# Kernel optimization log

Measured on AMD Instinct MI355X. Metric: run time of the kernel, lower is better.

Reference implementation:

```python
import jax, jax.numpy as jnp
import numpy as np
import math

EMBED_DIM = 512
NUM_HEADS = 8
B, T = 1, 4096

def setup_inputs() -> dict:
    key = jax.random.key(0)
    ks = jax.random.split(key, 12)
    D = EMBED_DIM
    s = 1.0 / math.sqrt(D)
    inp = {
        "x": jax.random.normal(ks[0], (B, T, D), dtype=jnp.float32),
        "ln1_scale": jnp.ones((D,), jnp.float32),
        "ln1_bias": jnp.zeros((D,), jnp.float32),
        "Wq": jax.random.normal(ks[1], (D, D), jnp.float32) * s,
        "bq": jnp.zeros((D,), jnp.float32),
        "Wk": jax.random.normal(ks[2], (D, D), jnp.float32) * s,
        "bk": jnp.zeros((D,), jnp.float32),
        "Wv": jax.random.normal(ks[3], (D, D), jnp.float32) * s,
        "bv": jnp.zeros((D,), jnp.float32),
        "Wo": jax.random.normal(ks[4], (D, D), jnp.float32) * s,
        "bo": jnp.zeros((D,), jnp.float32),
        "ln2_scale": jnp.ones((D,), jnp.float32),
        "ln2_bias": jnp.zeros((D,), jnp.float32),
        "W1": jax.random.normal(ks[5], (D, 4 * D), jnp.float32) * s,
        "b1": jnp.zeros((4 * D,), jnp.float32),
        "W2": jax.random.normal(ks[6], (4 * D, D), jnp.float32) * (1.0 / math.sqrt(4 * D)),
        "b2": jnp.zeros((D,), jnp.float32),
    }
    return inp

def _layernorm(x, scale, bias, eps=1e-6):
    mu = jnp.mean(x, axis=-1, keepdims=True)
    var = jnp.mean(jnp.square(x - mu), axis=-1, keepdims=True)
    return (x - mu) * jax.lax.rsqrt(var + eps) * scale + bias

def reference(x, ln1_scale, ln1_bias, Wq, bq, Wk, bk, Wv, bv, Wo, bo,
              ln2_scale, ln2_bias, W1, b1, W2, b2):
    Bb, Tt, D = x.shape
    H = NUM_HEADS
    hd = D // H
    residual = x
    h = _layernorm(x, ln1_scale, ln1_bias)
    q = (h @ Wq + bq).reshape(Bb, Tt, H, hd).transpose(0, 2, 1, 3)
    k = (h @ Wk + bk).reshape(Bb, Tt, H, hd).transpose(0, 2, 1, 3)
    v = (h @ Wv + bv).reshape(Bb, Tt, H, hd).transpose(0, 2, 1, 3)
    # [B,H,T,T] scores (naive attention as in the original module)
    scores = jnp.einsum('bhqd,bhkd->bhqk', q, k) / math.sqrt(hd)
    probs = jax.nn.softmax(scores, axis=-1)
    out = jnp.einsum('bhqk,bhkd->bhqd', probs, v).transpose(0, 2, 1, 3).reshape(Bb, Tt, D)
    h = out @ Wo + bo  # dropout deterministic -> identity
    x = h + residual
    residual = x
    h = _layernorm(x, ln2_scale, ln2_bias)
    h = jax.nn.gelu(h @ W1 + b1, approximate=True)
    h = h @ W2 + b2
    return h + residual
```

## Files before the change

kernel.cpp:

```cpp
#include <hip/hip_runtime.h>
#include <hip/hip_bf16.h>
#include <stdint.h>

typedef __bf16 bf16;
typedef __bf16 bf16x4 __attribute__((ext_vector_type(4)));
typedef __bf16 bf16x8 __attribute__((ext_vector_type(8)));
typedef float  f32x4  __attribute__((ext_vector_type(4)));
typedef float  f32x16 __attribute__((ext_vector_type(16)));

#define MFMA16(A_, B_, C_) __builtin_amdgcn_mfma_f32_16x16x32_bf16((A_), (B_), (C_), 0, 0, 0)
#define MFMA32(A_, B_, C_) __builtin_amdgcn_mfma_f32_32x32x16_bf16((A_), (B_), (C_), 0, 0, 0)

#define QSCALE 0.1803368801111137f

__device__ __forceinline__ void gload_lds16(const void* g, void* l) {
  __builtin_amdgcn_global_load_lds(
      (const __attribute__((address_space(1))) unsigned int*)g,
      (__attribute__((address_space(3))) unsigned int*)l, 16, 0, 0);
}

__device__ __forceinline__ unsigned pk2(float lo, float hi_) {
  union { bf16 h[2]; unsigned u; } t;
  t.h[0] = (bf16)lo; t.h[1] = (bf16)hi_;
  return t.u;
}

__device__ __forceinline__ float fast_exp2(float x) {
#if __has_builtin(__builtin_amdgcn_exp2f)
  return __builtin_amdgcn_exp2f(x);
#else
  return exp2f(x);
#endif
}

__global__ __launch_bounds__(256) void prep(const float* __restrict__ Wq,
                                            const float* __restrict__ Wk,
                                            const float* __restrict__ Wv,
                                            const float* __restrict__ Wo,
                                            const float* __restrict__ W1,
                                            const float* __restrict__ W2,
                                            const float* __restrict__ bq,
                                            const float* __restrict__ bk,
                                            const float* __restrict__ bv,
                                            bf16* __restrict__ wqkvT, bf16* __restrict__ woT,
                                            bf16* __restrict__ w1T, bf16* __restrict__ w2T,
                                            float* __restrict__ bqkv) {
  const int b = blockIdx.x;
  if (b >= 768) {
    int i = (b - 768) * 256 + threadIdx.x;
    if (i < 1536)
      bqkv[i] = (i < 512) ? bq[i] * QSCALE : (i < 1024 ? bk[i - 512] : bv[i - 1024]);
    return;
  }
  const float* in; bf16* outp; int K, N, t; float sc = 1.f;
  if (b < 64)       { in = Wq; outp = wqkvT;              K = 512;  N = 512;  t = b;       sc = QSCALE; }
  else if (b < 128) { in = Wk; outp = wqkvT + 512 * 512;  K = 512;  N = 512;  t = b - 64;  }
  else if (b < 192) { in = Wv; outp = wqkvT + 1024 * 512; K = 512;  N = 512;  t = b - 128; }
  else if (b < 256) { in = Wo; outp = woT;                K = 512;  N = 512;  t = b - 192; }
  else if (b < 512) { in = W1; outp = w1T;                K = 512;  N = 2048; t = b - 256; }
  else              { in = W2; outp = w2T;                K = 2048; N = 512;  t = b - 512; }
  const int tx = K >> 6;
  const int k0 = (t % tx) * 64, n0 = (t / tx) * 64;
  __shared__ bf16 tile[64][72];
  const int tid = threadIdx.x;
#pragma unroll
  for (int s = 0; s < 16; ++s) {
    int j = tid + s * 256;
    int r = j >> 6, c = j & 63;
    tile[r][c] = (bf16)(in[(size_t)(k0 + r) * N + n0 + c] * sc);
  }
  __syncthreads();
#pragma unroll
  for (int s = 0; s < 16; ++s) {
    int j = tid + s * 256;
    int n = j >> 6, k = j & 63;
    outp[(size_t)(n0 + n) * K + k0 + k] = tile[k][n];
  }
}

__global__ __launch_bounds__(256) void ln_k(const float* __restrict__ x,
                                            const float* __restrict__ sc,
                                            const float* __restrict__ bi,
                                            bf16* __restrict__ out) {
  const int w = threadIdx.x >> 6, l = threadIdx.x & 63;
  const int row = blockIdx.x * 4 + w;
  const float4* xp = (const float4*)(x + (size_t)row * 512 + l * 8);
  float4 v0 = xp[0], v1 = xp[1];
  float xv[8] = {v0.x, v0.y, v0.z, v0.w, v1.x, v1.y, v1.z, v1.w};
  float s = 0.f, q = 0.f;
#pragma unroll
  for (int j = 0; j < 8; ++j) { s += xv[j]; q += xv[j] * xv[j]; }
#pragma unroll
  for (int m = 1; m < 64; m <<= 1) { s += __shfl_xor(s, m); q += __shfl_xor(q, m); }
  const float mean = s * (1.f / 512.f);
  const float var = q * (1.f / 512.f) - mean * mean;
  const float rstd = rsqrtf(var + 1e-6f);
  const float4* scp = (const float4*)(sc + l * 8);
  const float4* bip = (const float4*)(bi + l * 8);
  float4 s0 = scp[0], s1 = scp[1], b0 = bip[0], b1 = bip[1];
  float sv[8] = {s0.x, s0.y, s0.z, s0.w, s1.x, s1.y, s1.z, s1.w};
  float bv[8] = {b0.x, b0.y, b0.z, b0.w, b1.x, b1.y, b1.z, b1.w};
  bf16x8 ov;
#pragma unroll
  for (int j = 0; j < 8; ++j) ov[j] = (bf16)((xv[j] - mean) * rstd * sv[j] + bv[j]);
  *(bf16x8*)(out + (size_t)row * 512 + l * 8) = ov;
}

__global__ __launch_bounds__(256) void ln2_comb(const float* __restrict__ p0,
                                                const float* __restrict__ p1,
                                                const float* __restrict__ x,
                                                const float* __restrict__ bo,
                                                const float* __restrict__ sc,
                                                const float* __restrict__ bi,
                                                float* __restrict__ x2,
                                                bf16* __restrict__ h2) {
  const int w = threadIdx.x >> 6, l = threadIdx.x & 63;
  const int row = blockIdx.x * 4 + w;
  const size_t base = (size_t)row * 512 + l * 8;
  float xv[8];
#pragma unroll
  for (int j = 0; j < 2; ++j) {
    float4 a = *(const float4*)(p0 + base + j * 4);
    float4 b = *(const float4*)(p1 + base + j * 4);
    float4 c = *(const float4*)(x + base + j * 4);
    float4 d = *(const float4*)(bo + l * 8 + j * 4);
    xv[j * 4 + 0] = a.x + b.x + c.x + d.x;
    xv[j * 4 + 1] = a.y + b.y + c.y + d.y;
    xv[j * 4 + 2] = a.z + b.z + c.z + d.z;
    xv[j * 4 + 3] = a.w + b.w + c.w + d.w;
  }
  *(float4*)(x2 + base) = make_float4(xv[0], xv[1], xv[2], xv[3]);
  *(float4*)(x2 + base + 4) = make_float4(xv[4], xv[5], xv[6], xv[7]);
  float s = 0.f, q = 0.f;
#pragma unroll
  for (int j = 0; j < 8; ++j) { s += xv[j]; q += xv[j] * xv[j]; }
#pragma unroll
  for (int m = 1; m < 64; m <<= 1) { s += __shfl_xor(s, m); q += __shfl_xor(q, m); }
  const float mean = s * (1.f / 512.f);
  const float var = q * (1.f / 512.f) - mean * mean;
  const float rstd = rsqrtf(var + 1e-6f);
  const float4* scp = (const float4*)(sc + l * 8);
  const float4* bip = (const float4*)(bi + l * 8);
  float4 s0 = scp[0], s1 = scp[1], b0 = bip[0], b1 = bip[1];
  float sv[8] = {s0.x, s0.y, s0.z, s0.w, s1.x, s1.y, s1.z, s1.w};
  float bv[8] = {b0.x, b0.y, b0.z, b0.w, b1.x, b1.y, b1.z, b1.w};
  bf16x8 ov;
#pragma unroll
  for (int j = 0; j < 8; ++j) ov[j] = (bf16)((xv[j] - mean) * rstd * sv[j] + bv[j]);
  *(bf16x8*)(h2 + base) = ov;
}

__global__ __launch_bounds__(256) void final_comb(const float* __restrict__ parts, int nsplit,
                                                  const float* __restrict__ b2,
                                                  const float* __restrict__ x2,
                                                  float* __restrict__ outp) {
  const int i4 = blockIdx.x * 256 + threadIdx.x;
  const size_t off = (size_t)i4 * 4;
  float4 acc = *(const float4*)(x2 + off);
  float4 bb = *(const float4*)(b2 + (off & 511));
  acc.x += bb.x; acc.y += bb.y; acc.z += bb.z; acc.w += bb.w;
  for (int z = 0; z < nsplit; ++z) {
    float4 p = *(const float4*)(parts + (size_t)z * 4096 * 512 + off);
    acc.x += p.x; acc.y += p.y; acc.z += p.z; acc.w += p.w;
  }
  *(float4*)(outp + off) = acc;
}

template <int EPI>
__global__ __launch_bounds__(256) void gemm_bt(const bf16* __restrict__ A,
                                               const bf16* __restrict__ Bt,
                                               const float* __restrict__ bias,
                                               const float* __restrict__ res,
                                               void* __restrict__ outp,
                                               bf16* __restrict__ k2,
                                               bf16* __restrict__ v2,
                                               int M, int N, int K) {
  __shared__ bf16 a_lds[2][128 * 64];
  __shared__ bf16 b_lds[2][128 * 64];
  const int m0 = blockIdx.x * 128, n0 = blockIdx.y * 128;
  const int tid = threadIdx.x, l = tid & 63, w = tid >> 6;
  const int wm = w >> 1, wn = w & 1;
  const int lc = l & 15, g = l >> 4;
  const int srow = l >> 3;
  const int cs = (l & 7) ^ srow;

  const bf16* ag = A + (size_t)(m0 + w * 8 + srow) * K + cs * 8;
  const bf16* bg = Bt + (size_t)(n0 + w * 8 + srow) * K + cs * 8;
  const size_t rstep = (size_t)32 * K;

#define GSTAGE(B_)                                                       \
  do {                                                                   \
    _Pragma("unroll")                                                    \
    for (int r_ = 0; r_ < 4; ++r_) {                                     \
      gload_lds16(ag + r_ * rstep, (char*)a_lds[B_] + (r_ * 32 + w * 8) * 128); \
      gload_lds16(bg + r_ * rstep, (char*)b_lds[B_] + (r_ * 32 + w * 8) * 128); \
    }                                                                    \
    ag += 64; bg += 64;                                                  \
  } while (0)

  f32x4 acc[4][4] = {};
  const int kiters = K >> 6;
  GSTAGE(0);
  __syncthreads();
  for (int kt = 0; kt < kiters; ++kt) {
    const int cur = kt & 1;
    if (kt + 1 < kiters) GSTAGE(cur ^ 1);
    const bf16* ab = a_lds[cur];
    const bf16* bb2 = b_lds[cur];
#pragma unroll
    for (int kk = 0; kk < 2; ++kk) {
      bf16x8 af[4], bfr[4];
#pragma unroll
      for (int i = 0; i < 4; ++i) {
        const int sw = ((kk * 4 + g) ^ (lc & 7)) * 8;
        af[i]  = *(const bf16x8*)(ab + (wm * 64 + i * 16 + lc) * 64 + sw);
        bfr[i] = *(const bf16x8*)(bb2 + (wn * 64 + i * 16 + lc) * 64 + sw);
      }
#pragma unroll
      for (int mi = 0; mi < 4; ++mi)
#pragma unroll
        for (int ni = 0; ni < 4; ++ni)
          acc[mi][ni] = MFMA16(af[mi], bfr[ni], acc[mi][ni]);
    }
    __syncthreads();
  }
#undef GSTAGE

#pragma unroll
  for (int mi = 0; mi < 4; ++mi)
#pragma unroll
    for (int ni = 0; ni < 4; ++ni) {
      const int col = n0 + wn * 64 + ni * 16 + lc;
      const float bb = bias[col];
#pragma unroll
      for (int i = 0; i < 4; ++i) {
        const int row = m0 + wm * 64 + mi * 16 + g * 4 + i;
        float v = acc[mi][ni][i] + bb;
        if constexpr (EPI == 1) {
          ((float*)outp)[(size_t)row * N + col] = v + res[(size_t)row * N + col];
        } else if constexpr (EPI == 2) {
          float t = -2.3022077697f * (v + 0.044715f * v * v * v);
          float gl = v / (1.f + fast_exp2(t));
          ((bf16*)outp)[(size_t)row * N + col] = (bf16)gl;
        } else {
          const bf16 bv16 = (bf16)v;
          if (col < 512) {
            ((bf16*)outp)[(size_t)row * 512 + col] = bv16;
          } else if (col < 1024) {
            const int hd = (col - 512) >> 6, d = col & 63;
            k2[(size_t)hd * 262144 + (size_t)row * 64 + d] = bv16;
          } else {
            const int hd = (col - 1024) >> 6, d = col & 63;
            v2[(size_t)hd * 262144 + (size_t)(row >> 5) * 2048 + d * 32 + (row & 31)] = bv16;
          }
        }
      }
    }
}

__global__ __launch_bounds__(256) void gemm_skp(const bf16* __restrict__ A,
                                                const bf16* __restrict__ Bt,
                                                float* __restrict__ parts,
                                                int M, int N, int Kstride, int Kc) {
  __shared__ bf16 a_lds[2][128 * 64];
  __shared__ bf16 b_lds[2][128 * 64];
  const int m0 = blockIdx.x * 128, n0 = blockIdx.y * 128, kz = blockIdx.z;
  A += (size_t)kz * Kc;
  Bt += (size_t)kz * Kc;
  float* outp = parts + (size_t)kz * M * N;
  const int tid = threadIdx.x, l = tid & 63, w = tid >> 6;
  const int wm = w >> 1, wn = w & 1;
  const int lc = l & 15, g = l >> 4;
  const int srow = l >> 3;
  const int cs = (l & 7) ^ srow;

  const bf16* ag = A + (size_t)(m0 + w * 8 + srow) * Kstride + cs * 8;
  const bf16* bg = Bt + (size_t)(n0 + w * 8 + srow) * Kstride + cs * 8;
  const size_t rstep = (size_t)32 * Kstride;

#define GSTAGE(B_)                                                       \
  do {                                                                   \
    _Pragma("unroll")                                                    \
    for (int r_ = 0; r_ < 4; ++r_) {                                     \
      gload_lds16(ag + r_ * rstep, (char*)a_lds[B_] + (r_ * 32 + w * 8) * 128); \
      gload_lds16(bg + r_ * rstep, (char*)b_lds[B_] + (r_ * 32 + w * 8) * 128); \
    }                                                                    \
    ag += 64; bg += 64;                                                  \
  } while (0)

  f32x4 acc[4][4] = {};
  const int kiters = Kc >> 6;
  GSTAGE(0);
  __syncthreads();
  for (int kt = 0; kt < kiters; ++kt) {
    const int cur = kt & 1;
    if (kt + 1 < kiters) GSTAGE(cur ^ 1);
    const bf16* ab = a_lds[cur];
    const bf16* bb2 = b_lds[cur];
#pragma unroll
    for (int kk = 0; kk < 2; ++kk) {
      bf16x8 af[4], bfr[4];
#pragma unroll
      for (int i = 0; i < 4; ++i) {
        const int sw = ((kk * 4 + g) ^ (lc & 7)) * 8;
        af[i]  = *(const bf16x8*)(ab + (wm * 64 + i * 16 + lc) * 64 + sw);
        bfr[i] = *(const bf16x8*)(bb2 + (wn * 64 + i * 16 + lc) * 64 + sw);
      }
#pragma unroll
      for (int mi = 0; mi < 4; ++mi)
#pragma unroll
        for (int ni = 0; ni < 4; ++ni)
          acc[mi][ni] = MFMA16(af[mi], bfr[ni], acc[mi][ni]);
    }
    __syncthreads();
  }
#undef GSTAGE

#pragma unroll
  for (int mi = 0; mi < 4; ++mi)
#pragma unroll
    for (int ni = 0; ni < 4; ++ni) {
      const int col = n0 + wn * 64 + ni * 16 + lc;
#pragma unroll
      for (int i = 0; i < 4; ++i) {
        const int row = m0 + wm * 64 + mi * 16 + g * 4 + i;
        outp[(size_t)row * N + col] = acc[mi][ni][i];
      }
    }
}

__global__ __launch_bounds__(256, 4) void attn_k(const bf16* __restrict__ q2,
                                                 const bf16* __restrict__ k2,
                                                 const bf16* __restrict__ v2,
                                                 bf16* __restrict__ opart,
                                                 float* __restrict__ lpart) {
  const int bid = blockIdx.x;
  const int head = bid & 7;
  const int qt = (bid >> 3) & 63;
  const int ks = bid >> 9;
  const int w = threadIdx.x >> 6, l = threadIdx.x & 63;
  const int hi = l >> 5, l5 = l & 31;
  const int pair = w >> 1, wq = w & 1;

  __shared__ __align__(16) char smem[32768];
  char* kt_l = smem + pair * 16384;
  char* vt_l = kt_l + 8192;

  const int qrow0 = qt * 64 + wq * 32;
  const bf16* qb = q2 + (size_t)(qrow0 + l5) * 512 + head * 64;
  bf16x8 qf[4];
#pragma unroll
  for (int cc = 0; cc < 4; ++cc) qf[cc] = *(const bf16x8*)(qb + cc * 16 + hi * 8);

  const int kstart = ks * 2048 + pair * 1024;

  const int lr = l >> 3;
  const int lc3 = (l & 7) ^ lr;
  const char* kg = (const char*)k2 + (size_t)head * 524288 + (size_t)kstart * 128 +
                   (wq * 16 + lr) * 128 + lc3 * 16;
  const char* vg = (const char*)v2 + (size_t)head * 524288 + (size_t)(kstart >> 5) * 4096 +
                   (lc3 >> 2) * 2048 + (wq * 16 + lr) * 64 + (lc3 & 3) * 16;
  const int kdst = wq * 2048;

#define STAGE(B_)                                                            \
  do {                                                                       \
    gload_lds16(kg,        kt_l + (B_) * 4096 + kdst);                       \
    gload_lds16(kg + 1024, kt_l + (B_) * 4096 + kdst + 1024);                \
    gload_lds16(vg,        vt_l + (B_) * 4096 + kdst);                       \
    gload_lds16(vg + 512,  vt_l + (B_) * 4096 + kdst + 1024);                \
    kg += 4096; vg += 4096;                                                  \
  } while (0)

  STAGE(0);
  __syncthreads();

  f32x16 o0 = {}, o1 = {};
  float psum = 0.f;
  const int swl = l5 & 7;
  const char* kbase = kt_l + l5 * 128;
  const char* vbase = vt_l + l5 * 128;

  for (int t = 0; t < 32; ++t) {
    const int cur = t & 1;
    if (t < 31) STAGE(cur ^ 1);

    __builtin_amdgcn_s_setprio(1);
    f32x16 s = {};
#pragma unroll
    for (int cc = 0; cc < 4; ++cc) {
      bf16x8 kf = *(const bf16x8*)(kbase + cur * 4096 + ((cc * 2 + hi) ^ swl) * 16);
      s = MFMA32(kf, qf[cc], s);
    }
    __builtin_amdgcn_s_setprio(0);

#pragma unroll
    for (int c = 0; c < 2; ++c) {
      float p[8];
#pragma unroll
      for (int j = 0; j < 8; ++j) p[j] = fast_exp2(s[c * 8 + j]);
      psum += ((p[0] + p[1]) + (p[2] + p[3])) + ((p[4] + p[5]) + (p[6] + p[7]));
      unsigned X = pk2(p[0], p[1]), X2 = pk2(p[2], p[3]);
      unsigned Y = pk2(p[4], p[5]), Y2 = pk2(p[6], p[7]);
      asm volatile("v_permlane32_swap_b32 %0, %1" : "+v"(X), "+v"(Y));
      asm volatile("v_permlane32_swap_b32 %0, %1" : "+v"(X2), "+v"(Y2));
      union { unsigned wd[4]; bf16x8 v; } pa;
      pa.wd[0] = X; pa.wd[1] = X2; pa.wd[2] = Y; pa.wd[3] = Y2;
      bf16x8 vf0 = *(const bf16x8*)(vbase + cur * 4096 + ((c * 2 + hi) ^ swl) * 16);
      bf16x8 vf1 = *(const bf16x8*)(vbase + cur * 4096 + ((4 + c * 2 + hi) ^ swl) * 16);
      __builtin_amdgcn_s_setprio(1);
      o0 = MFMA32(vf0, pa.v, o0);
      o1 = MFMA32(vf1, pa.v, o1);
      __builtin_amdgcn_s_setprio(0);
    }
    __syncthreads();
  }
#undef STAGE

  float* comb = (float*)smem;
  if (w >= 2) {
    float* cb = comb + ((w - 2) * 64 + l) * 33;
#pragma unroll
    for (int r = 0; r < 16; ++r) { cb[r] = o0[r]; cb[16 + r] = o1[r]; }
    cb[32] = psum;
  }
  __syncthreads();
  if (w < 2) {
    const float* cb = comb + (w * 64 + l) * 33;
#pragma unroll
    for (int r = 0; r < 16; ++r) { o0[r] += cb[r]; o1[r] += cb[16 + r]; }
    psum += cb[32];
    const float lsum = psum + __shfl_xor(psum, 32);
    bf16* ob = opart + (size_t)ks * 4096 * 512 + (size_t)(qrow0 + l5) * 512 + head * 64;
#pragma unroll
    for (int dt = 0; dt < 2; ++dt)
#pragma unroll
      for (int rg = 0; rg < 4; ++rg) {
        bf16x4 vv;
#pragma unroll
        for (int e = 0; e < 4; ++e) {
          const float ov = (dt == 0) ? o0[rg * 4 + e] : o1[rg * 4 + e];
          vv[e] = (bf16)ov;
        }
        *(bf16x4*)(ob + dt * 32 + rg * 8 + hi * 4) = vv;
      }
    if (hi == 0) lpart[(ks * 8 + head) * 4096 + qrow0 + l5] = lsum;
  }
}

__global__ __launch_bounds__(256) void attn_comb(const bf16* __restrict__ op,
                                                 const float* __restrict__ lp,
                                                 bf16* __restrict__ ob) {
  const int idx = blockIdx.x * 256 + threadIdx.x;
  const int t = idx >> 6, c8 = idx & 63;
  const int head = c8 >> 3;
  const size_t o = (size_t)t * 512 + c8 * 8;
  bf16x8 a = *(const bf16x8*)(op + o);
  bf16x8 b = *(const bf16x8*)(op + 2097152 + o);
  const float inv = 1.f / (lp[head * 4096 + t] + lp[32768 + head * 4096 + t]);
  bf16x8 r;
#pragma unroll
  for (int j = 0; j < 8; ++j) r[j] = (bf16)(((float)a[j] + (float)b[j]) * inv);
  *(bf16x8*)(ob + o) = r;
}

extern "C" void kernel_launch(void* const* d_in, const int* in_sizes, int n_in,
                              void* d_out, int out_size, void* d_ws, size_t ws_size,
                              hipStream_t stream) {
  const float* x    = (const float*)d_in[0];
  const float* ln1s = (const float*)d_in[1];
  const float* ln1b = (const float*)d_in[2];
  const float* Wq   = (const float*)d_in[3];
  const float* bq   = (const float*)d_in[4];
  const float* Wk   = (const float*)d_in[5];
  const float* bk   = (const float*)d_in[6];
  const float* Wv   = (const float*)d_in[7];
  const float* bv   = (const float*)d_in[8];
  const float* Wo   = (const float*)d_in[9];
  const float* bo   = (const float*)d_in[10];
  const float* ln2s = (const float*)d_in[11];
  const float* ln2b = (const float*)d_in[12];
  const float* W1   = (const float*)d_in[13];
  const float* b1   = (const float*)d_in[14];
  const float* W2   = (const float*)d_in[15];
  const float* b2   = (const float*)d_in[16];
  float* out = (float*)d_out;

  char* ws = (char*)d_ws;
  bf16*  wqkvT = (bf16*)(ws + 0);
  bf16*  woT   = (bf16*)(ws + 1572864);
  bf16*  w1T   = (bf16*)(ws + 2097152);
  bf16*  w2T   = (bf16*)(ws + 4194304);
  float* bqkv  = (float*)(ws + 6291456);
  float* lpart = (float*)(ws + 6299648);
  bf16*  opart = (bf16*)(ws + 6561792);
  float* x2    = (float*)(ws + 6561792);
  bf16*  h     = (bf16*)(ws + 14950400);
  bf16*  q2    = (bf16*)(ws + 19144704);
  bf16*  k2    = (bf16*)(ws + 23339008);
  bf16*  v2    = (bf16*)(ws + 27533312);
  bf16*  attnb = h;
  bf16*  h2    = h;
  float* wop   = (float*)(ws + 19144704);
  bf16*  gbuf  = (bf16*)(ws + 19144704);
  float* f2p   = (float*)(ws + 35921920);
  const size_t need4 = 35921920 + 4ull * 8388608;
  const size_t need2 = 35921920 + 2ull * 8388608;

  prep<<<774, 256, 0, stream>>>(Wq, Wk, Wv, Wo, W1, W2, bq, bk, bv,
                                wqkvT, woT, w1T, w2T, bqkv);

  ln_k<<<1024, 256, 0, stream>>>(x, ln1s, ln1b, h);
  gemm_bt<3><<<dim3(32, 12), 256, 0, stream>>>(h, wqkvT, bqkv, nullptr, q2, k2, v2,
                                               4096, 1536, 512);
  attn_k<<<1024, 256, 0, stream>>>(q2, k2, v2, opart, lpart);
  attn_comb<<<1024, 256, 0, stream>>>(opart, lpart, attnb);
  gemm_skp<<<dim3(32, 4, 2), 256, 0, stream>>>(attnb, woT, wop, 4096, 512, 512, 256);
  ln2_comb<<<1024, 256, 0, stream>>>(wop, wop + 4096 * 512, x, bo, ln2s, ln2b, x2, h2);
  gemm_bt<2><<<dim3(32, 16), 256, 0, stream>>>(h2, w1T, b1, nullptr, gbuf, nullptr, nullptr,
                                               4096, 2048, 512);
  if (ws_size >= need4) {
    gemm_skp<<<dim3(32, 4, 4), 256, 0, stream>>>(gbuf, w2T, f2p, 4096, 512, 2048, 512);
    final_comb<<<2048, 256, 0, stream>>>(f2p, 4, b2, x2, out);
  } else if (ws_size >= need2) {
    gemm_skp<<<dim3(32, 4, 2), 256, 0, stream>>>(gbuf, w2T, f2p, 4096, 512, 2048, 1024);
    final_comb<<<2048, 256, 0, stream>>>(f2p, 2, b2, x2, out);
  } else {
    gemm_bt<1><<<dim3(32, 4), 256, 0, stream>>>(gbuf, w2T, b2, x2, out, nullptr, nullptr,
                                                4096, 512, 2048);
  }
}
```

Measured before the change: 147.7 us.

## Switch GEMMs to 64x64 tiles with 32x32 MFMA, bf16 split-K partials, fused LN1

All GEMMs now use 64x64 block tiles, with each wave computing one 32x32x16 MFMA accumulator instead of 128x128 tiles built from 16x16 MFMAs. This gives more blocks, higher occupancy and vectorized epilogue stores. Split-K partials are stored as bf16 rather than fp32, which halves partial-sum traffic at some precision cost. LN1 is folded into the weight-prep launch to save a launch. The V transpose moves out of the QKV epilogue into a separate vtrans kernel, which costs an extra pass over V.

```diff
diff --git a/kernel.cpp b/kernel.cpp
--- a/kernel.cpp
+++ b/kernel.cpp
@@ -8,7 +8,6 @@
 typedef float  f32x4  __attribute__((ext_vector_type(4)));
 typedef float  f32x16 __attribute__((ext_vector_type(16)));
 
-#define MFMA16(A_, B_, C_) __builtin_amdgcn_mfma_f32_16x16x32_bf16((A_), (B_), (C_), 0, 0, 0)
 #define MFMA32(A_, B_, C_) __builtin_amdgcn_mfma_f32_32x32x16_bf16((A_), (B_), (C_), 0, 0, 0)
 
 #define QSCALE 0.1803368801111137f
@@ -33,19 +32,48 @@
 #endif
 }
 
-__global__ __launch_bounds__(256) void prep(const float* __restrict__ Wq,
-                                            const float* __restrict__ Wk,
-                                            const float* __restrict__ Wv,
-                                            const float* __restrict__ Wo,
-                                            const float* __restrict__ W1,
-                                            const float* __restrict__ W2,
-                                            const float* __restrict__ bq,
-                                            const float* __restrict__ bk,
-                                            const float* __restrict__ bv,
-                                            bf16* __restrict__ wqkvT, bf16* __restrict__ woT,
-                                            bf16* __restrict__ w1T, bf16* __restrict__ w2T,
-                                            float* __restrict__ bqkv) {
+__global__ __launch_bounds__(256) void prep_ln(const float* __restrict__ Wq,
+                                               const float* __restrict__ Wk,
+                                               const float* __restrict__ Wv,
+                                               const float* __restrict__ Wo,
+                                               const float* __restrict__ W1,
+                                               const float* __restrict__ W2,
+                                               const float* __restrict__ bq,
+                                               const float* __restrict__ bk,
+                                               const float* __restrict__ bv,
+                                               bf16* __restrict__ wqkvT, bf16* __restrict__ woT,
+                                               bf16* __restrict__ w1T, bf16* __restrict__ w2T,
+                                               float* __restrict__ bqkv,
+                                               const float* __restrict__ x,
+                                               const float* __restrict__ ln1s,
+                                               const float* __restrict__ ln1b,
+                                               bf16* __restrict__ h) {
   const int b = blockIdx.x;
+  if (b >= 774) {
+    const int w = threadIdx.x >> 6, l = threadIdx.x & 63;
+    const int row = (b - 774) * 4 + w;
+    const float4* xp = (const float4*)(x + (size_t)row * 512 + l * 8);
+    float4 v0 = xp[0], v1 = xp[1];
+    float xv[8] = {v0.x, v0.y, v0.z, v0.w, v1.x, v1.y, v1.z, v1.w};
+    float s = 0.f, q = 0.f;
+#pragma unroll
+    for (int j = 0; j < 8; ++j) { s += xv[j]; q += xv[j] * xv[j]; }
+#pragma unroll
+    for (int m = 1; m < 64; m <<= 1) { s += __shfl_xor(s, m); q += __shfl_xor(q, m); }
+    const float mean = s * (1.f / 512.f);
+    const float var = q * (1.f / 512.f) - mean * mean;
+    const float rstd = rsqrtf(var + 1e-6f);
+    const float4* scp = (const float4*)(ln1s + l * 8);
+    const float4* bip = (const float4*)(ln1b + l * 8);
+    float4 s0 = scp[0], s1 = scp[1], b0 = bip[0], b1 = bip[1];
+    float sv[8] = {s0.x, s0.y, s0.z, s0.w, s1.x, s1.y, s1.z, s1.w};
+    float bvv[8] = {b0.x, b0.y, b0.z, b0.w, b1.x, b1.y, b1.z, b1.w};
+    bf16x8 ov;
+#pragma unroll
+    for (int j = 0; j < 8; ++j) ov[j] = (bf16)((xv[j] - mean) * rstd * sv[j] + bvv[j]);
+    *(bf16x8*)(h + (size_t)row * 512 + l * 8) = ov;
+    return;
+  }
   if (b >= 768) {
     int i = (b - 768) * 256 + threadIdx.x;
     if (i < 1536)
@@ -78,36 +106,8 @@
   }
 }
 
-__global__ __launch_bounds__(256) void ln_k(const float* __restrict__ x,
-                                            const float* __restrict__ sc,
-                                            const float* __restrict__ bi,
-                                            bf16* __restrict__ out) {
-  const int w = threadIdx.x >> 6, l = threadIdx.x & 63;
-  const int row = blockIdx.x * 4 + w;
-  const float4* xp = (const float4*)(x + (size_t)row * 512 + l * 8);
-  float4 v0 = xp[0], v1 = xp[1];
-  float xv[8] = {v0.x, v0.y, v0.z, v0.w, v1.x, v1.y, v1.z, v1.w};
-  float s = 0.f, q = 0.f;
-#pragma unroll
-  for (int j = 0; j < 8; ++j) { s += xv[j]; q += xv[j] * xv[j]; }
-#pragma unroll
-  for (int m = 1; m < 64; m <<= 1) { s += __shfl_xor(s, m); q += __shfl_xor(q, m); }
-  const float mean = s * (1.f / 512.f);
-  const float var = q * (1.f / 512.f) - mean * mean;
-  const float rstd = rsqrtf(var + 1e-6f);
-  const float4* scp = (const float4*)(sc + l * 8);
-  const float4* bip = (const float4*)(bi + l * 8);
-  float4 s0 = scp[0], s1 = scp[1], b0 = bip[0], b1 = bip[1];
-  float sv[8] = {s0.x, s0.y, s0.z, s0.w, s1.x, s1.y, s1.z, s1.w};
-  float bv[8] = {b0.x, b0.y, b0.z, b0.w, b1.x, b1.y, b1.z, b1.w};
-  bf16x8 ov;
-#pragma unroll
-  for (int j = 0; j < 8; ++j) ov[j] = (bf16)((xv[j] - mean) * rstd * sv[j] + bv[j]);
-  *(bf16x8*)(out + (size_t)row * 512 + l * 8) = ov;
-}
-
-__global__ __launch_bounds__(256) void ln2_comb(const float* __restrict__ p0,
-                                                const float* __restrict__ p1,
+__global__ __launch_bounds__(256) void ln2_comb(const bf16* __restrict__ p0,
+                                                const bf16* __restrict__ p1,
                                                 const float* __restrict__ x,
                                                 const float* __restrict__ bo,
                                                 const float* __restrict__ sc,
@@ -117,17 +117,17 @@
   const int w = threadIdx.x >> 6, l = threadIdx.x & 63;
   const int row = blockIdx.x * 4 + w;
   const size_t base = (size_t)row * 512 + l * 8;
+  bf16x8 a = *(const bf16x8*)(p0 + base);
+  bf16x8 b = *(const bf16x8*)(p1 + base);
   float xv[8];
 #pragma unroll
   for (int j = 0; j < 2; ++j) {
-    float4 a = *(const float4*)(p0 + base + j * 4);
-    float4 b = *(const float4*)(p1 + base + j * 4);
     float4 c = *(const float4*)(x + base + j * 4);
     float4 d = *(const float4*)(bo + l * 8 + j * 4);
-    xv[j * 4 + 0] = a.x + b.x + c.x + d.x;
-    xv[j * 4 + 1] = a.y + b.y + c.y + d.y;
-    xv[j * 4 + 2] = a.z + b.z + c.z + d.z;
-    xv[j * 4 + 3] = a.w + b.w + c.w + d.w;
+    xv[j * 4 + 0] = (float)a[j * 4 + 0] + (float)b[j * 4 + 0] + c.x + d.x;
+    xv[j * 4 + 1] = (float)a[j * 4 + 1] + (float)b[j * 4 + 1] + c.y + d.y;
+    xv[j * 4 + 2] = (float)a[j * 4 + 2] + (float)b[j * 4 + 2] + c.z + d.z;
+    xv[j * 4 + 3] = (float)a[j * 4 + 3] + (float)b[j * 4 + 3] + c.w + d.w;
   }
   *(float4*)(x2 + base) = make_float4(xv[0], xv[1], xv[2], xv[3]);
   *(float4*)(x2 + base + 4) = make_float4(xv[4], xv[5], xv[6], xv[7]);
@@ -143,190 +143,205 @@
   const float4* bip = (const float4*)(bi + l * 8);
   float4 s0 = scp[0], s1 = scp[1], b0 = bip[0], b1 = bip[1];
   float sv[8] = {s0.x, s0.y, s0.z, s0.w, s1.x, s1.y, s1.z, s1.w};
-  float bv[8] = {b0.x, b0.y, b0.z, b0.w, b1.x, b1.y, b1.z, b1.w};
+  float bvv[8] = {b0.x, b0.y, b0.z, b0.w, b1.x, b1.y, b1.z, b1.w};
   bf16x8 ov;
 #pragma unroll
-  for (int j = 0; j < 8; ++j) ov[j] = (bf16)((xv[j] - mean) * rstd * sv[j] + bv[j]);
+  for (int j = 0; j < 8; ++j) ov[j] = (bf16)((xv[j] - mean) * rstd * sv[j] + bvv[j]);
   *(bf16x8*)(h2 + base) = ov;
 }
 
-__global__ __launch_bounds__(256) void final_comb(const float* __restrict__ parts, int nsplit,
+__global__ __launch_bounds__(256) void final_comb(const bf16* __restrict__ parts, int nsplit,
                                                   const float* __restrict__ b2,
                                                   const float* __restrict__ x2,
                                                   float* __restrict__ outp) {
-  const int i4 = blockIdx.x * 256 + threadIdx.x;
-  const size_t off = (size_t)i4 * 4;
-  float4 acc = *(const float4*)(x2 + off);
-  float4 bb = *(const float4*)(b2 + (off & 511));
-  acc.x += bb.x; acc.y += bb.y; acc.z += bb.z; acc.w += bb.w;
+  const int i8 = blockIdx.x * 256 + threadIdx.x;
+  const size_t off = (size_t)i8 * 8;
+  float acc[8];
+  float4 xa = *(const float4*)(x2 + off);
+  float4 xb = *(const float4*)(x2 + off + 4);
+  float4 ba = *(const float4*)(b2 + (off & 511));
+  float4 bb = *(const float4*)(b2 + ((off & 511) + 4));
+  acc[0] = xa.x + ba.x; acc[1] = xa.y + ba.y; acc[2] = xa.z + ba.z; acc[3] = xa.w + ba.w;
+  acc[4] = xb.x + bb.x; acc[5] = xb.y + bb.y; acc[6] = xb.z + bb.z; acc[7] = xb.w + bb.w;
   for (int z = 0; z < nsplit; ++z) {
-    float4 p = *(const float4*)(parts + (size_t)z * 4096 * 512 + off);
-    acc.x += p.x; acc.y += p.y; acc.z += p.z; acc.w += p.w;
-  }
-  *(float4*)(outp + off) = acc;
+    bf16x8 p = *(const bf16x8*)(parts + (size_t)z * 2097152 + off);
+#pragma unroll
+    for (int j = 0; j < 8; ++j) acc[j] += (float)p[j];
+  }
+  *(float4*)(outp + off) = make_float4(acc[0], acc[1], acc[2], acc[3]);
+  *(float4*)(outp + off + 4) = make_float4(acc[4], acc[5], acc[6], acc[7]);
 }
 
 template <int EPI>
-__global__ __launch_bounds__(256) void gemm_bt(const bf16* __restrict__ A,
-                                               const bf16* __restrict__ Bt,
-                                               const float* __restrict__ bias,
-                                               const float* __restrict__ res,
-                                               void* __restrict__ outp,
-                                               bf16* __restrict__ k2,
-                                               bf16* __restrict__ v2,
-                                               int M, int N, int K) {
-  __shared__ bf16 a_lds[2][128 * 64];
-  __shared__ bf16 b_lds[2][128 * 64];
-  const int m0 = blockIdx.x * 128, n0 = blockIdx.y * 128;
+__global__ __launch_bounds__(256, 4) void gemm32(const bf16* __restrict__ A,
+                                                 const bf16* __restrict__ Bt,
+                                                 const float* __restrict__ bias,
+                                                 const float* __restrict__ res,
+                                                 void* __restrict__ outp,
+                                                 bf16* __restrict__ k2,
+                                                 bf16* __restrict__ vd,
+                                                 int M, int N, int K) {
+  __shared__ bf16 a_lds[2][64 * 64];
+  __shared__ bf16 b_lds[2][64 * 64];
+  const int m0 = blockIdx.x * 64, n0 = blockIdx.y * 64;
   const int tid = threadIdx.x, l = tid & 63, w = tid >> 6;
   const int wm = w >> 1, wn = w & 1;
-  const int lc = l & 15, g = l >> 4;
-  const int srow = l >> 3;
-  const int cs = (l & 7) ^ srow;
-
-  const bf16* ag = A + (size_t)(m0 + w * 8 + srow) * K + cs * 8;
-  const bf16* bg = Bt + (size_t)(n0 + w * 8 + srow) * K + cs * 8;
-  const size_t rstep = (size_t)32 * K;
-
-#define GSTAGE(B_)                                                       \
-  do {                                                                   \
-    _Pragma("unroll")                                                    \
-    for (int r_ = 0; r_ < 4; ++r_) {                                     \
-      gload_lds16(ag + r_ * rstep, (char*)a_lds[B_] + (r_ * 32 + w * 8) * 128); \
-      gload_lds16(bg + r_ * rstep, (char*)b_lds[B_] + (r_ * 32 + w * 8) * 128); \
-    }                                                                    \
-    ag += 64; bg += 64;                                                  \
+  const int hi = l >> 5, l5 = l & 31;
+  const int lr = l >> 3;
+  const int cs = (l & 7) ^ (lr & 7);
+  const int swl = l5 & 7;
+
+  const bf16* ag = A + (size_t)(m0 + w * 16 + lr) * K + cs * 8;
+  const bf16* bg = Bt + (size_t)(n0 + w * 16 + lr) * K + cs * 8;
+  const size_t r8 = (size_t)8 * K;
+
+#define GS32(B_)                                                   \
+  do {                                                             \
+    gload_lds16(ag,      (char*)a_lds[B_] + (w * 16) * 128);       \
+    gload_lds16(ag + r8, (char*)a_lds[B_] + (w * 16 + 8) * 128);   \
+    gload_lds16(bg,      (char*)b_lds[B_] + (w * 16) * 128);       \
+    gload_lds16(bg + r8, (char*)b_lds[B_] + (w * 16 + 8) * 128);   \
+    ag += 64; bg += 64;                                            \
   } while (0)
 
-  f32x4 acc[4][4] = {};
+  f32x16 acc = {};
   const int kiters = K >> 6;
-  GSTAGE(0);
+  GS32(0);
   __syncthreads();
   for (int kt = 0; kt < kiters; ++kt) {
     const int cur = kt & 1;
-    if (kt + 1 < kiters) GSTAGE(cur ^ 1);
-    const bf16* ab = a_lds[cur];
-    const bf16* bb2 = b_lds[cur];
-#pragma unroll
-    for (int kk = 0; kk < 2; ++kk) {
-      bf16x8 af[4], bfr[4];
-#pragma unroll
-      for (int i = 0; i < 4; ++i) {
-        const int sw = ((kk * 4 + g) ^ (lc & 7)) * 8;
-        af[i]  = *(const bf16x8*)(ab + (wm * 64 + i * 16 + lc) * 64 + sw);
-        bfr[i] = *(const bf16x8*)(bb2 + (wn * 64 + i * 16 + lc) * 64 + sw);
-      }
-#pragma unroll
-      for (int mi = 0; mi < 4; ++mi)
-#pragma unroll
-        for (int ni = 0; ni < 4; ++ni)
-          acc[mi][ni] = MFMA16(af[mi], bfr[ni], acc[mi][ni]);
+    if (kt + 1 < kiters) GS32(cur ^ 1);
+    const bf16* ab = a_lds[cur] + (wm * 32 + l5) * 64;
+    const bf16* bb = b_lds[cur] + (wn * 32 + l5) * 64;
+#pragma unroll
+    for (int kk = 0; kk < 4; ++kk) {
+      bf16x8 af = *(const bf16x8*)(ab + ((kk * 2 + hi) ^ swl) * 8);
+      bf16x8 bf_ = *(const bf16x8*)(bb + ((kk * 2 + hi) ^ swl) * 8);
+      acc = MFMA32(bf_, af, acc);
     }
     __syncthreads();
   }
-#undef GSTAGE
-
-#pragma unroll
-  for (int mi = 0; mi < 4; ++mi)
-#pragma unroll
-    for (int ni = 0; ni < 4; ++ni) {
-      const int col = n0 + wn * 64 + ni * 16 + lc;
-      const float bb = bias[col];
-#pragma unroll
-      for (int i = 0; i < 4; ++i) {
-        const int row = m0 + wm * 64 + mi * 16 + g * 4 + i;
-        float v = acc[mi][ni][i] + bb;
-        if constexpr (EPI == 1) {
-          ((float*)outp)[(size_t)row * N + col] = v + res[(size_t)row * N + col];
-        } else if constexpr (EPI == 2) {
-          float t = -2.3022077697f * (v + 0.044715f * v * v * v);
-          float gl = v / (1.f + fast_exp2(t));
-          ((bf16*)outp)[(size_t)row * N + col] = (bf16)gl;
-        } else {
-          const bf16 bv16 = (bf16)v;
-          if (col < 512) {
-            ((bf16*)outp)[(size_t)row * 512 + col] = bv16;
-          } else if (col < 1024) {
-            const int hd = (col - 512) >> 6, d = col & 63;
-            k2[(size_t)hd * 262144 + (size_t)row * 64 + d] = bv16;
-          } else {
-            const int hd = (col - 1024) >> 6, d = col & 63;
-            v2[(size_t)hd * 262144 + (size_t)(row >> 5) * 2048 + d * 32 + (row & 31)] = bv16;
-          }
-        }
+#undef GS32
+
+  const int row = m0 + wm * 32 + l5;
+#pragma unroll
+  for (int rg = 0; rg < 4; ++rg) {
+    const int cb = n0 + wn * 32 + rg * 8 + hi * 4;
+    float4 bb4 = *(const float4*)(bias + cb);
+    float v[4];
+    v[0] = acc[rg * 4 + 0] + bb4.x;
+    v[1] = acc[rg * 4 + 1] + bb4.y;
+    v[2] = acc[rg * 4 + 2] + bb4.z;
+    v[3] = acc[rg * 4 + 3] + bb4.w;
+    if constexpr (EPI == 1) {
+      float4 rr = *(const float4*)(res + (size_t)row * N + cb);
+      *(float4*)((float*)outp + (size_t)row * N + cb) =
+          make_float4(v[0] + rr.x, v[1] + rr.y, v[2] + rr.z, v[3] + rr.w);
+    } else if constexpr (EPI == 2) {
+      bf16x4 o;
+#pragma unroll
+      for (int e = 0; e < 4; ++e) {
+        float t = -2.3022077697f * (v[e] + 0.044715f * v[e] * v[e] * v[e]);
+        o[e] = (bf16)(v[e] / (1.f + fast_exp2(t)));
+      }
+      *(bf16x4*)((bf16*)outp + (size_t)row * N + cb) = o;
+    } else {
+      bf16x4 o;
+#pragma unroll
+      for (int e = 0; e < 4; ++e) o[e] = (bf16)v[e];
+      if (n0 < 512) {
+        *(bf16x4*)((bf16*)outp + (size_t)row * 512 + cb) = o;
+      } else if (n0 < 1024) {
+        const int hd = (n0 - 512) >> 6, d = cb & 63;
+        *(bf16x4*)(k2 + (size_t)hd * 262144 + (size_t)row * 64 + d) = o;
+      } else {
+        const int hd = (n0 - 1024) >> 6, d = cb & 63;
+        *(bf16x4*)(vd + (size_t)hd * 262144 + (size_t)row * 64 + d) = o;
       }
     }
-}
-
-__global__ __launch_bounds__(256) void gemm_skp(const bf16* __restrict__ A,
-                                                const bf16* __restrict__ Bt,
-                                                float* __restrict__ parts,
-                                                int M, int N, int Kstride, int Kc) {
-  __shared__ bf16 a_lds[2][128 * 64];
-  __shared__ bf16 b_lds[2][128 * 64];
-  const int m0 = blockIdx.x * 128, n0 = blockIdx.y * 128, kz = blockIdx.z;
+  }
+}
+
+__global__ __launch_bounds__(256, 4) void gemm32_skp(const bf16* __restrict__ A,
+                                                     const bf16* __restrict__ Bt,
+                                                     bf16* __restrict__ parts,
+                                                     int M, int N, int Kstride, int Kc) {
+  __shared__ bf16 a_lds[2][64 * 64];
+  __shared__ bf16 b_lds[2][64 * 64];
+  const int m0 = blockIdx.x * 64, n0 = blockIdx.y * 64, kz = blockIdx.z;
   A += (size_t)kz * Kc;
   Bt += (size_t)kz * Kc;
-  float* outp = parts + (size_t)kz * M * N;
+  bf16* outp = parts + (size_t)kz * M * N;
   const int tid = threadIdx.x, l = tid & 63, w = tid >> 6;
   const int wm = w >> 1, wn = w & 1;
-  const int lc = l & 15, g = l >> 4;
-  const int srow = l >> 3;
-  const int cs = (l & 7) ^ srow;
-
-  const bf16* ag = A + (size_t)(m0 + w * 8 + srow) * Kstride + cs * 8;
-  const bf16* bg = Bt + (size_t)(n0 + w * 8 + srow) * Kstride + cs * 8;
-  const size_t rstep = (size_t)32 * Kstride;
-
-#define GSTAGE(B_)                                                       \
-  do {                                                                   \
-    _Pragma("unroll")                                                    \
-    for (int r_ = 0; r_ < 4; ++r_) {                                     \
-      gload_lds16(ag + r_ * rstep, (char*)a_lds[B_] + (r_ * 32 + w * 8) * 128); \
-      gload_lds16(bg + r_ * rstep, (char*)b_lds[B_] + (r_ * 32 + w * 8) * 128); \
-    }                                                                    \
-    ag += 64; bg += 64;                                                  \
+  const int hi = l >> 5, l5 = l & 31;
+  const int lr = l >> 3;
+  const int cs = (l & 7) ^ (lr & 7);
+  const int swl = l5 & 7;
+
+  const bf16* ag = A + (size_t)(m0 + w * 16 + lr) * Kstride + cs * 8;
+  const bf16* bg = Bt + (size_t)(n0 + w * 16 + lr) * Kstride + cs * 8;
+  const size_t r8 = (size_t)8 * Kstride;
+
+#define GS32(B_)                                                   \
+  do {                                                             \
+    gload_lds16(ag,      (char*)a_lds[B_] + (w * 16) * 128);       \
+    gload_lds16(ag + r8, (char*)a_lds[B_] + (w * 16 + 8) * 128);   \
+    gload_lds16(bg,      (char*)b_lds[B_] + (w * 16) * 128);       \
+    gload_lds16(bg + r8, (char*)b_lds[B_] + (w * 16 + 8) * 128);   \
+    ag += 64; bg += 64;                                            \
   } while (0)
 
-  f32x4 acc[4][4] = {};
+  f32x16 acc = {};
   const int kiters = Kc >> 6;
-  GSTAGE(0);
+  GS32(0);
   __syncthreads();
   for (int kt = 0; kt < kiters; ++kt) {
     const int cur = kt & 1;
-    if (kt + 1 < kiters) GSTAGE(cur ^ 1);
-    const bf16* ab = a_lds[cur];
-    const bf16* bb2 = b_lds[cur];
-#pragma unroll
-    for (int kk = 0; kk < 2; ++kk) {
-      bf16x8 af[4], bfr[4];
-#pragma unroll
-      for (int i = 0; i < 4; ++i) {
-        const int sw = ((kk * 4 + g) ^ (lc & 7)) * 8;
-        af[i]  = *(const bf16x8*)(ab + (wm * 64 + i * 16 + lc) * 64 + sw);
-        bfr[i] = *(const bf16x8*)(bb2 + (wn * 64 + i * 16 + lc) * 64 + sw);
-      }
-#pragma unroll
-      for (int mi = 0; mi < 4; ++mi)
-#pragma unroll
-        for (int ni = 0; ni < 4; ++ni)
-          acc[mi][ni] = MFMA16(af[mi], bfr[ni], acc[mi][ni]);
+    if (kt + 1 < kiters) GS32(cur ^ 1);
+    const bf16* ab = a_lds[cur] + (wm * 32 + l5) * 64;
+    const bf16* bb = b_lds[cur] + (wn * 32 + l5) * 64;
+#pragma unroll
+    for (int kk = 0; kk < 4; ++kk) {
+      bf16x8 af = *(const bf16x8*)(ab + ((kk * 2 + hi) ^ swl) * 8);
+      bf16x8 bf_ = *(const bf16x8*)(bb + ((kk * 2 + hi) ^ swl) * 8);
+      acc = MFMA32(bf_, af, acc);
     }
     __syncthreads();
   }
-#undef GSTAGE
-
-#pragma unroll
-  for (int mi = 0; mi < 4; ++mi)
-#pragma unroll
-    for (int ni = 0; ni < 4; ++ni) {
-      const int col = n0 + wn * 64 + ni * 16 + lc;
-#pragma unroll
-      for (int i = 0; i < 4; ++i) {
-        const int row = m0 + wm * 64 + mi * 16 + g * 4 + i;
-        outp[(size_t)row * N + col] = acc[mi][ni][i];
-      }
-    }
+#undef GS32
+
+  const int row = m0 + wm * 32 + l5;
+#pragma unroll
+  for (int rg = 0; rg < 4; ++rg) {
+    const int cb = n0 + wn * 32 + rg * 8 + hi * 4;
+    bf16x4 o;
+#pragma unroll
+    for (int e = 0; e < 4; ++e) o[e] = (bf16)acc[rg * 4 + e];
+    *(bf16x4*)(outp + (size_t)row * N + cb) = o;
+  }
+}
+
+__global__ __launch_bounds__(256) void vtrans(const bf16* __restrict__ vd,
+                                              bf16* __restrict__ v2) {
+  __shared__ bf16 tile[64][72];
+  const int t0 = blockIdx.x * 64;
+  const int head = blockIdx.y;
+  const int tid = threadIdx.x;
+#pragma unroll
+  for (int s = 0; s < 16; ++s) {
+    int j = tid + s * 256;
+    int t = j >> 6, d = j & 63;
+    tile[t][d] = vd[(size_t)head * 262144 + (size_t)(t0 + t) * 64 + d];
+  }
+  __syncthreads();
+#pragma unroll
+  for (int s = 0; s < 16; ++s) {
+    int j = tid + s * 256;
+    int d = j >> 6, t = j & 63;
+    v2[(size_t)head * 262144 + (size_t)((t0 >> 5) + (t >> 5)) * 2048 + d * 32 + (t & 31)] =
+        tile[t][d];
+  }
 }
 
 __global__ __launch_bounds__(256, 4) void attn_k(const bf16* __restrict__ q2,
@@ -498,34 +513,34 @@
   bf16*  q2    = (bf16*)(ws + 19144704);
   bf16*  k2    = (bf16*)(ws + 23339008);
   bf16*  v2    = (bf16*)(ws + 27533312);
+  bf16*  vd    = (bf16*)(ws + 31727616);
   bf16*  attnb = h;
   bf16*  h2    = h;
-  float* wop   = (float*)(ws + 19144704);
+  bf16*  wop   = (bf16*)(ws + 19144704);
   bf16*  gbuf  = (bf16*)(ws + 19144704);
-  float* f2p   = (float*)(ws + 35921920);
-  const size_t need4 = 35921920 + 4ull * 8388608;
-  const size_t need2 = 35921920 + 2ull * 8388608;
-
-  prep<<<774, 256, 0, stream>>>(Wq, Wk, Wv, Wo, W1, W2, bq, bk, bv,
-                                wqkvT, woT, w1T, w2T, bqkv);
-
-  ln_k<<<1024, 256, 0, stream>>>(x, ln1s, ln1b, h);
-  gemm_bt<3><<<dim3(32, 12), 256, 0, stream>>>(h, wqkvT, bqkv, nullptr, q2, k2, v2,
-                                               4096, 1536, 512);
+  bf16*  f2p   = (bf16*)(ws + 35921920);
+  const size_t need4 = 35921920 + 4ull * 4194304;
+  const size_t need2 = 35921920 + 2ull * 4194304;
+
+  prep_ln<<<1798, 256, 0, stream>>>(Wq, Wk, Wv, Wo, W1, W2, bq, bk, bv,
+                                    wqkvT, woT, w1T, w2T, bqkv, x, ln1s, ln1b, h);
+  gemm32<3><<<dim3(64, 24), 256, 0, stream>>>(h, wqkvT, bqkv, nullptr, q2, k2, vd,
+                                              4096, 1536, 512);
+  vtrans<<<dim3(64, 8), 256, 0, stream>>>(vd, v2);
   attn_k<<<1024, 256, 0, stream>>>(q2, k2, v2, opart, lpart);
   attn_comb<<<1024, 256, 0, stream>>>(opart, lpart, attnb);
-  gemm_skp<<<dim3(32, 4, 2), 256, 0, stream>>>(attnb, woT, wop, 4096, 512, 512, 256);
-  ln2_comb<<<1024, 256, 0, stream>>>(wop, wop + 4096 * 512, x, bo, ln2s, ln2b, x2, h2);
-  gemm_bt<2><<<dim3(32, 16), 256, 0, stream>>>(h2, w1T, b1, nullptr, gbuf, nullptr, nullptr,
-                                               4096, 2048, 512);
+  gemm32_skp<<<dim3(64, 8, 2), 256, 0, stream>>>(attnb, woT, wop, 4096, 512, 512, 256);
+  ln2_comb<<<1024, 256, 0, stream>>>(wop, wop + 2097152, x, bo, ln2s, ln2b, x2, h2);
+  gemm32<2><<<dim3(64, 32), 256, 0, stream>>>(h2, w1T, b1, nullptr, gbuf, nullptr, nullptr,
+                                              4096, 2048, 512);
   if (ws_size >= need4) {
-    gemm_skp<<<dim3(32, 4, 4), 256, 0, stream>>>(gbuf, w2T, f2p, 4096, 512, 2048, 512);
-    final_comb<<<2048, 256, 0, stream>>>(f2p, 4, b2, x2, out);
+    gemm32_skp<<<dim3(64, 8, 4), 256, 0, stream>>>(gbuf, w2T, f2p, 4096, 512, 2048, 512);
+    final_comb<<<1024, 256, 0, stream>>>(f2p, 4, b2, x2, out);
   } else if (ws_size >= need2) {
-    gemm_skp<<<dim3(32, 4, 2), 256, 0, stream>>>(gbuf, w2T, f2p, 4096, 512, 2048, 1024);
-    final_comb<<<2048, 256, 0, stream>>>(f2p, 2, b2, x2, out);
+    gemm32_skp<<<dim3(64, 8, 2), 256, 0, stream>>>(gbuf, w2T, f2p, 4096, 512, 2048, 1024);
+    final_comb<<<1024, 256, 0, stream>>>(f2p, 2, b2, x2, out);
   } else {
-    gemm_bt<1><<<dim3(32, 4), 256, 0, stream>>>(gbuf, w2T, b2, x2, out, nullptr, nullptr,
-                                                4096, 512, 2048);
-  }
-}
+    gemm32<1><<<dim3(64, 8), 256, 0, stream>>>(gbuf, w2T, b2, x2, out, nullptr, nullptr,
+                                               4096, 512, 2048);
+  }
+}
```

Measured after the change: 150.8 us. 2.1% more time.
